# Kernel tuning notes

Measured on AMD Instinct MI355X. Metric: run time of the kernel, lower is better.

Reference implementation:

```python
import jax, jax.numpy as jnp
import numpy as np

N = 100000   # nodes
E = 1600000  # edges
F = 128      # in = hidden channels
L = 4        # num GCN layers
G = 512      # graphs in batch
OUT = 10     # classes
EPS = 1e-5


def setup_inputs() -> dict:
    key = jax.random.key(0)
    ks = jax.random.split(key, 12)
    x = jax.random.normal(ks[0], (N, F), dtype=jnp.float32)
    edge_index = jax.random.randint(ks[1], (2, E), 0, N, dtype=jnp.int64)
    batch = jnp.sort(jax.random.randint(ks[2], (N,), 0, G, dtype=jnp.int64))
    s = 1.0 / np.sqrt(F)
    Ws = jax.random.uniform(ks[3], (L, F, F), jnp.float32, -s, s)
    bs = jax.random.uniform(ks[4], (L, F), jnp.float32, -s, s)
    gammas = jnp.ones((L, F), jnp.float32)
    betas = jnp.zeros((L, F), jnp.float32)
    s1 = 1.0 / np.sqrt(F * L)
    W1 = jax.random.uniform(ks[5], (F * L, F), jnp.float32, -s1, s1)
    b1 = jax.random.uniform(ks[6], (F,), jnp.float32, -s1, s1)
    g1 = jnp.ones((F,), jnp.float32)
    bt1 = jnp.zeros((F,), jnp.float32)
    s2 = 1.0 / np.sqrt(F)
    W2 = jax.random.uniform(ks[7], (F, OUT), jnp.float32, -s2, s2)
    b2 = jax.random.uniform(ks[8], (OUT,), jnp.float32, -s2, s2)
    return {"x": x, "edge_index": edge_index, "batch": batch, "Ws": Ws, "bs": bs,
            "gammas": gammas, "betas": betas, "W1": W1, "b1": b1, "g1": g1,
            "bt1": bt1, "W2": W2, "b2": b2}


def _batch_norm(x, g, b):
    # training-mode BatchNorm1d over the node dim (biased variance)
    mu = jnp.mean(x, axis=0)
    var = jnp.var(x, axis=0)
    return (x - mu) * jax.lax.rsqrt(var + EPS) * g + b


def reference(x, edge_index, batch, Ws, bs, gammas, betas, W1, b1, g1, bt1, W2, b2):
    row, col = edge_index[0], edge_index[1]
    # GCN normalization (add_self_loops=False since normalize=True)
    deg = jax.ops.segment_sum(jnp.ones((E,), x.dtype), col, num_segments=N)
    dinv = jnp.where(deg > 0, jax.lax.rsqrt(deg), 0.0)
    norm = dinv[row] * dinv[col]  # [E]
    pooled = []
    h = x
    for t in range(L):
        hw = h @ Ws[t]                                    # [N, F]
        msg = norm[:, None] * hw[row]                     # gather  [E, F]
        h = jax.ops.segment_sum(msg, col, num_segments=N) + bs[t]  # scatter [N, F]
        h = jax.nn.relu(h)
        h = _batch_norm(h, gammas[t], betas[t])
        pooled.append(jax.ops.segment_sum(h, batch, num_segments=G))  # [G, F]
    z = jnp.concatenate(pooled, axis=1)                   # [G, L*F]
    z = z @ W1 + b1
    z = _batch_norm(z, g1, bt1)
    z = jax.nn.relu(z)
    return z @ W2 + b2                                    # [G, OUT]
```

## Files before the change

### kernel.cpp

```cpp
#include <hip/hip_runtime.h>

#define NN 100000
#define EE 1600000
#define FF 128
#define LL 4
#define GG 512
#define OUTC 10
#define EPSF 1e-5f
#define NSCB ((NN + 255) / 256)

#define NPW 8
#define AGG_WAVES ((NN + NPW - 1) / NPW)
#define AGG_BLOCKS ((AGG_WAVES + 3) / 4)

typedef __attribute__((ext_vector_type(8))) short short8;
typedef __attribute__((ext_vector_type(4))) float f32x4;

__device__ inline unsigned bf16rne(float f) {
  unsigned u = __float_as_uint(f);
  return (u + 0x7fffu + ((u >> 16) & 1u)) >> 16;
}
__device__ inline unsigned packbf(float lo, float hi) {
  return bf16rne(lo) | (bf16rne(hi) << 16);
}
__device__ inline float bflo(unsigned u) { return __uint_as_float(u << 16); }
__device__ inline float bfhi(unsigned u) { return __uint_as_float(u & 0xffff0000u); }


__global__ __launch_bounds__(256) void k_deg(const int* __restrict__ col, int* __restrict__ deg) {
  int e = blockIdx.x * 256 + threadIdx.x;
  if (e < EE) atomicAdd(&deg[col[e]], 1);
}

__global__ __launch_bounds__(256) void k_bsum(const int* __restrict__ deg,
                                              int* __restrict__ bsum,
                                              float* __restrict__ dinv) {
  int i = blockIdx.x * 256 + threadIdx.x;
  int v = (i < NN) ? deg[i] : 0;
  if (i < NN) dinv[i] = v > 0 ? rsqrtf((float)v) : 0.0f;
#pragma unroll
  for (int off = 32; off > 0; off >>= 1) v += __shfl_down(v, off, 64);
  __shared__ int ws[4];
  if ((threadIdx.x & 63) == 0) ws[threadIdx.x >> 6] = v;
  __syncthreads();
  if (threadIdx.x == 0) bsum[blockIdx.x] = ws[0] + ws[1] + ws[2] + ws[3];
}

__global__ __launch_bounds__(256) void k_rowptr(const int* __restrict__ deg,
                                                const int* __restrict__ bsum,
                                                int* __restrict__ rowptr) {
  __shared__ int sb[512];
  __shared__ int sd[256];
  const int t = threadIdx.x;
  sb[t]       = (t < NSCB) ? bsum[t] : 0;
  sb[t + 256] = (t + 256 < NSCB) ? bsum[t + 256] : 0;
  __syncthreads();
#pragma unroll
  for (int off = 1; off < 512; off <<= 1) {
    int v0 = (t >= off) ? sb[t - off] : 0;
    int v1 = sb[t + 256 - off];
    __syncthreads();
    sb[t] += v0;
    sb[t + 256] += v1;
    __syncthreads();
  }
  const int bpre = (blockIdx.x == 0) ? 0 : sb[blockIdx.x - 1];
  const int i = blockIdx.x * 256 + t;
  const int d = (i < NN) ? deg[i] : 0;
  sd[t] = d;
  __syncthreads();
#pragma unroll
  for (int off = 1; off < 256; off <<= 1) {
    int v = (t >= off) ? sd[t - off] : 0;
    __syncthreads();
    sd[t] += v;
    __syncthreads();
  }
  if (i < NN) rowptr[i] = bpre + sd[t] - d;
  if (blockIdx.x == 0 && t == 0) rowptr[NN] = EE;
}

__global__ __launch_bounds__(256) void k_fill(const int* __restrict__ ei,
                                              const int* __restrict__ rowptr,
                                              int* __restrict__ cnt,
                                              const float* __restrict__ dinv,
                                              int2* __restrict__ ecw) {
  int e = blockIdx.x * 256 + threadIdx.x;
  if (e >= EE) return;
  int r = ei[e];
  int cl = ei[EE + e];
  int slot = rowptr[cl] + atomicAdd(&cnt[cl], 1);
  ecw[slot] = make_int2(r, __float_as_int(dinv[r] * dinv[cl]));
}


__global__ __launch_bounds__(256) void k_cvt(const float* __restrict__ x,
                                             const int* __restrict__ batch,
                                             unsigned* __restrict__ Ab,
                                             int* __restrict__ gstart) {
  int i = blockIdx.x * 256 + threadIdx.x;
  if (i < NN * 64) {
    float2 v = *(const float2*)(x + (size_t)i * 2);
    Ab[i] = packbf(v.x, v.y);
  }
  if (i < NN) {
    int b = batch[i];
    if (i == 0) {
      for (int g = 0; g <= b; ++g) gstart[g] = 0;
    } else {
      int bp = batch[i - 1];
      for (int g = bp + 1; g <= b; ++g) gstart[g] = i;
    }
    if (i == NN - 1) {
      for (int g = b + 1; g <= GG; ++g) gstart[g] = NN;
    }
  }
}

__global__ __launch_bounds__(256) void k_wcvt(const float* __restrict__ W,
                                              uint4* __restrict__ Wf) {
  int tid = blockIdx.x * 256 + threadIdx.x;
  int lane = tid & 63;
  int which = (tid >> 6) & 1;
  int ct = (tid >> 7) & 7;
  int kc = tid >> 10;
  int n = ct * 16 + (lane & 15);
  int k0 = kc * 32 + (lane >> 4) * 8;
  unsigned h[8];
#pragma unroll
  for (int j = 0; j < 8; ++j) {
    float w = W[(k0 + j) * 128 + n];
    unsigned hb = bf16rne(w);
    if (which == 0) {
      h[j] = hb;
    } else {
      float hf = __uint_as_float(hb << 16);
      h[j] = bf16rne(w - hf);
    }
  }
  uint4 o;
  o.x = h[0] | (h[1] << 16);
  o.y = h[2] | (h[3] << 16);
  o.z = h[4] | (h[5] << 16);
  o.w = h[6] | (h[7] << 16);
  Wf[tid] = o;
}

__global__ __launch_bounds__(256) void k_post(const float* __restrict__ bnbuf,
                                              const float* __restrict__ gamma,
                                              const float* __restrict__ beta,
                                              float* __restrict__ bnsc,
                                              const float* __restrict__ Wnext,
                                              uint4* __restrict__ Wf,
                                              float* __restrict__ baseo) {
  __shared__ float ssc[256];
  const int t = threadIdx.x;
  if (t < 128) {
    float mu = bnbuf[t] * (1.0f / NN);
    float var = bnbuf[128 + t] * (1.0f / NN) - mu * mu;
    float inv = rsqrtf(var + EPSF);
    float sc = gamma[t] * inv;
    float sh = beta[t] - mu * sc;
    ssc[t] = sc;
    ssc[128 + t] = sh;
    if (blockIdx.x == 0) {
      bnsc[t] = sc;
      bnsc[128 + t] = sh;
    }
  }
  __syncthreads();
  if (gridDim.x == 1) return;
  if (blockIdx.x < 16) {
    int tid = blockIdx.x * 256 + t;
    int lane = tid & 63;
    int which = (tid >> 6) & 1;
    int ct = (tid >> 7) & 7;
    int kc = tid >> 10;
    int n = ct * 16 + (lane & 15);
    int k0 = kc * 32 + (lane >> 4) * 8;
    unsigned h[8];
#pragma unroll
    for (int j = 0; j < 8; ++j) {
      float w = Wnext[(k0 + j) * 128 + n] * ssc[k0 + j];
      unsigned hb = bf16rne(w);
      if (which == 0) {
        h[j] = hb;
      } else {
        float hf = __uint_as_float(hb << 16);
        h[j] = bf16rne(w - hf);
      }
    }
    uint4 o;
    o.x = h[0] | (h[1] << 16);
    o.y = h[2] | (h[3] << 16);
    o.z = h[4] | (h[5] << 16);
    o.w = h[6] | (h[7] << 16);
    Wf[tid] = o;
  } else if (t < 128) {
    float acc = 0.f;
    for (int k = 0; k < 128; ++k) acc = fmaf(ssc[128 + k], Wnext[k * 128 + t], acc);
    baseo[t] = acc;
  }
}

__global__ __launch_bounds__(256) void k_mm(const unsigned* __restrict__ Ab,
                                            const uint4* __restrict__ Wf,
                                            unsigned* __restrict__ Bb) {
  const int lane = threadIdx.x & 63;
  const int w = threadIdx.x >> 6;
  const int quad = lane >> 4;
  const int m = lane & 15;
  const int rowbase = blockIdx.x * 64 + w * 16;
  const int arow = min(rowbase + m, NN - 1);
  const uint4* A4 = (const uint4*)Ab;
  f32x4 acc[8];
#pragma unroll
  for (int ct = 0; ct < 8; ++ct) acc[ct] = (f32x4){0.f, 0.f, 0.f, 0.f};
#pragma unroll
  for (int kc = 0; kc < 4; ++kc) {
    uint4 av = A4[arow * 16 + kc * 4 + quad];
    short8 af = *(short8*)&av;
#pragma unroll
    for (int ct = 0; ct < 8; ++ct) {
      uint4 bh = Wf[((kc * 8 + ct) * 2 + 0) * 64 + lane];
      uint4 bl = Wf[((kc * 8 + ct) * 2 + 1) * 64 + lane];
      acc[ct] = __builtin_amdgcn_mfma_f32_16x16x32_bf16(af, *(short8*)&bh, acc[ct], 0, 0, 0);
      acc[ct] = __builtin_amdgcn_mfma_f32_16x16x32_bf16(af, *(short8*)&bl, acc[ct], 0, 0, 0);
    }
  }
#pragma unroll
  for (int ct = 0; ct < 8; ++ct) {
#pragma unroll
    for (int r = 0; r < 4; ++r) {
      float v = acc[ct][r];
      float vo = __shfl_xor(v, 1);
      int row = rowbase + quad * 4 + r;
      if ((lane & 1) == 0 && row < NN) {
        Bb[row * 64 + ct * 8 + (m >> 1)] = packbf(v, vo);
      }
    }
  }
}

__global__ __launch_bounds__(256) void k_agg(const unsigned* __restrict__ Bb,
                                             const int* __restrict__ rowptr,
                                             const int2* __restrict__ ecw,
                                             const float* __restrict__ bias,
                                             const float* __restrict__ base,
                                             const int* __restrict__ batch,
                                             unsigned* __restrict__ Ar,
                                             float* __restrict__ bnbuf,
                                             float* __restrict__ pooledt) {
  const int lane = threadIdx.x & 63;
  const int wave = threadIdx.x >> 6;
  const int c = lane * 2;
  const int gwave = blockIdx.x * 4 + wave;
  const int n0 = gwave * NPW;
  const float2 bv = *(const float2*)(bias + c);
  const float2 basev = *(const float2*)(base + c);
  float s0 = 0.f, s1 = 0.f, q0 = 0.f, q1 = 0.f;
  __shared__ int srp[4][NPW + 1];
  __shared__ int2 sstage[4][64];
  if (n0 < NN) {
    const int nn = min(NPW, NN - n0);
    if (lane <= nn) srp[wave][lane] = rowptr[n0 + lane];
    int bsp = (lane < nn) ? batch[n0 + lane] : 0;
    float ax0 = 0.f, ax1 = 0.f, ay0 = 0.f, ay1 = 0.f, sw = 0.f;
    float px = 0.f, py = 0.f;
    int gprev = -1;
    auto finalize = [&](int node) {
      float rx = fmaxf(fmaf(sw, basev.x, ax0 + ax1) + bv.x, 0.f);
      float ry = fmaxf(fmaf(sw, basev.y, ay0 + ay1) + bv.y, 0.f);
      Ar[(size_t)(n0 + node) * 64 + lane] = packbf(rx, ry);
      s0 += rx; s1 += ry;
      q0 = fmaf(rx, rx, q0); q1 = fmaf(ry, ry, q1);
      int g = __shfl(bsp, node);
      if (g != gprev) {
        if (gprev >= 0) {
          atomicAdd(&pooledt[(size_t)gprev * 512 + c], px);
          atomicAdd(&pooledt[(size_t)gprev * 512 + c + 1], py);
        }
        gprev = g; px = 0.f; py = 0.f;
      }
      px += rx; py += ry;
      ax0 = 0.f; ax1 = 0.f; ay0 = 0.f; ay1 = 0.f; sw = 0.f;
    };
    const int beg = __builtin_amdgcn_readfirstlane(srp[wave][0]);
    const int endall = __builtin_amdgcn_readfirstlane(srp[wave][nn]);
    int cn = 0;
    while (cn < nn && __builtin_amdgcn_readfirstlane(srp[wave][cn + 1]) == beg) {
      finalize(cn);
      ++cn;
    }
    int nend = (cn < nn) ? __builtin_amdgcn_readfirstlane(srp[wave][cn + 1]) : 0x7fffffff;
    int2 stage = (beg + lane < endall) ? ecw[beg + lane] : make_int2(0, 0);
    for (int base_e = beg; base_e < endall; base_e += 64) {
      sstage[wave][lane] = stage;
      const int nb = base_e + 64;
      if (nb < endall) {
        stage = (nb + lane < endall) ? ecw[nb + lane] : make_int2(0, 0);
      }
      int2 ewA[16], ewB[16];
#pragma unroll
      for (int j = 0; j < 16; ++j) ewA[j] = sstage[wave][j];

#define PROC(G, CUR, NXT, PREF)                                               \
  if (base_e + (G) * 16 < endall) {                                           \
    if (PREF) {                                                               \
      _Pragma("unroll")                                                       \
      for (int j = 0; j < 16; ++j) NXT[j] = sstage[wave][((G) + 1) * 16 + j]; \
    }                                                                         \
    unsigned us[16];                                                          \
    _Pragma("unroll")                                                         \
    for (int j = 0; j < 16; ++j) {                                            \
      const int sj = __builtin_amdgcn_readfirstlane(CUR[j].x);                \
      us[j] = Bb[((size_t)(unsigned)sj << 6) + (unsigned)lane];               \
    }                                                                         \
    _Pragma("unroll")                                                         \
    for (int j = 0; j < 16; ++j) {                                            \
      const float wj = __int_as_float(CUR[j].y);                              \
      sw += wj;                                                               \
      if (j & 1) {                                                            \
        ax1 = fmaf(wj, bflo(us[j]), ax1);                                     \
        ay1 = fmaf(wj, bfhi(us[j]), ay1);                                     \
      } else {                                                                \
        ax0 = fmaf(wj, bflo(us[j]), ax0);                                     \
        ay0 = fmaf(wj, bfhi(us[j]), ay0);                                     \
      }                                                                       \
      const int e1 = base_e + (G) * 16 + j + 1;                               \
      if (e1 == nend) {                                                       \
        finalize(cn); ++cn;                                                   \
        nend = (cn < nn) ? __builtin_amdgcn_readfirstlane(srp[wave][cn + 1])  \
                         : 0x7fffffff;                                        \
        while (cn < nn && nend == e1) {                                       \
          finalize(cn); ++cn;                                                 \
          nend = (cn < nn)                                                    \
                     ? __builtin_amdgcn_readfirstlane(srp[wave][cn + 1])      \
                     : 0x7fffffff;                                            \
        }                                                                     \
      }                                                                       \
    }                                                                         \
  }

      PROC(0, ewA, ewB, true)
      PROC(1, ewB, ewA, true)
      PROC(2, ewA, ewB, true)
      PROC(3, ewB, ewA, false)
#undef PROC
    }
    if (gprev >= 0) {
      atomicAdd(&pooledt[(size_t)gprev * 512 + c], px);
      atomicAdd(&pooledt[(size_t)gprev * 512 + c + 1], py);
    }
  }
  __shared__ float sred[4][256];
  sred[wave][c] = s0;
  sred[wave][c + 1] = s1;
  sred[wave][128 + c] = q0;
  sred[wave][128 + c + 1] = q1;
  __syncthreads();
  const int t = threadIdx.x;
  float tot = sred[0][t] + sred[1][t] + sred[2][t] + sred[3][t];
  atomicAdd(&bnbuf[t], tot);
}


__global__ __launch_bounds__(128) void k_z1(const float* __restrict__ S,
                                            const float* __restrict__ bnscL,
                                            const int* __restrict__ gstart,
                                            const float* __restrict__ W1,
                                            const float* __restrict__ b1,
                                            float* __restrict__ z1) {
  __shared__ float sp[512];
  const int g = blockIdx.x;
  const float cntg = (float)(gstart[g + 1] - gstart[g]);
  for (int i = threadIdx.x; i < 512; i += 128) {
    int t = i >> 7, ch = i & 127;
    sp[i] = fmaf(bnscL[t * 256 + ch], S[(size_t)g * 512 + i], cntg * bnscL[t * 256 + 128 + ch]);
  }
  __syncthreads();
  const int c = threadIdx.x;
  float acc = b1[c];
  for (int j = 0; j < 512; ++j) acc = fmaf(sp[j], W1[j * 128 + c], acc);
  z1[(size_t)g * 128 + c] = acc;
}

__global__ __launch_bounds__(128) void k_zstat(const float* __restrict__ z1,
                                               const float* __restrict__ g1,
                                               const float* __restrict__ bt1,
                                               float* __restrict__ zsc) {
  const int c = threadIdx.x;
  float s = 0.f, q = 0.f;
  for (int g = 0; g < GG; ++g) {
    float v = z1[g * 128 + c];
    s += v;
    q = fmaf(v, v, q);
  }
  float mu = s * (1.0f / GG);
  float var = q * (1.0f / GG) - mu * mu;
  float inv = rsqrtf(var + EPSF);
  float sc = g1[c] * inv;
  zsc[c] = sc;
  zsc[128 + c] = bt1[c] - mu * sc;
}

__global__ __launch_bounds__(128) void k_out(const float* __restrict__ z1,
                                             const float* __restrict__ zsc,
                                             const float* __restrict__ W2,
                                             const float* __restrict__ b2,
                                             float* __restrict__ out) {
  __shared__ float zr[128];
  const int g = blockIdx.x;
  const int c = threadIdx.x;
  zr[c] = fmaxf(fmaf(z1[(size_t)g * 128 + c], zsc[c], zsc[128 + c]), 0.f);
  __syncthreads();
  if (c < OUTC) {
    float acc = b2[c];
    for (int k = 0; k < 128; ++k) acc = fmaf(zr[k], W2[k * OUTC + c], acc);
    out[(size_t)g * OUTC + c] = acc;
  }
}


extern "C" void kernel_launch(void* const* d_in, const int* in_sizes, int n_in,
                              void* d_out, int out_size, void* d_ws, size_t ws_size,
                              hipStream_t stream) {
  const float* x      = (const float*)d_in[0];
  const int*   ei     = (const int*)d_in[1];
  const int*   batch  = (const int*)d_in[2];
  const float* Ws     = (const float*)d_in[3];
  const float* bs     = (const float*)d_in[4];
  const float* gammas = (const float*)d_in[5];
  const float* betas  = (const float*)d_in[6];
  const float* W1     = (const float*)d_in[7];
  const float* b1     = (const float*)d_in[8];
  const float* g1     = (const float*)d_in[9];
  const float* bt1    = (const float*)d_in[10];
  const float* W2     = (const float*)d_in[11];
  const float* b2     = (const float*)d_in[12];
  float* out = (float*)d_out;

  char* ws = (char*)d_ws;
  size_t off = 0;
  auto alloc = [&](size_t bytes) -> void* {
    void* p = ws + off;
    off = (off + bytes + 255) & ~(size_t)255;
    return p;
  };
  int*   deg    = (int*)alloc((size_t)NN * 4);
  int*   cnt    = (int*)alloc((size_t)NN * 4);
  float* bnbuf  = (float*)alloc((size_t)LL * 256 * 4);
  float* pooled = (float*)alloc((size_t)GG * 512 * 4);
  float* zbase  = (float*)alloc(128 * 4);
  size_t zero_bytes = off;
  unsigned* Ar     = (unsigned*)alloc((size_t)NN * 64 * 4);
  unsigned* Ab     = (unsigned*)alloc((size_t)NN * 64 * 4);
  unsigned* Bb     = (unsigned*)alloc((size_t)NN * 64 * 4);
  int2*     ecw    = (int2*)alloc((size_t)EE * 8);
  float*    dinv   = (float*)alloc((size_t)NN * 4);
  int*      rowptr = (int*)alloc((size_t)(NN + 1) * 4);
  int*      bsum   = (int*)alloc((size_t)NSCB * 4);
  int*      gstart = (int*)alloc((size_t)(GG + 1) * 4);
  uint4*    Wf     = (uint4*)alloc((size_t)4096 * 16);
  float*    z1     = (float*)alloc((size_t)GG * FF * 4);
  float*    bnscL  = (float*)alloc((size_t)LL * 256 * 4);
  float*    basebf = (float*)alloc(128 * 4);
  float*    zsc    = (float*)alloc(256 * 4);
  (void)ws_size; (void)in_sizes; (void)n_in; (void)out_size;

  hipMemsetAsync(d_ws, 0, zero_bytes, stream);

  k_deg<<<(EE + 255) / 256, 256, 0, stream>>>(ei + EE, deg);
  k_bsum<<<NSCB, 256, 0, stream>>>(deg, bsum, dinv);
  k_rowptr<<<NSCB, 256, 0, stream>>>(deg, bsum, rowptr);
  k_fill<<<(EE + 255) / 256, 256, 0, stream>>>(ei, rowptr, cnt, dinv, ecw);
  k_cvt<<<(NN * 64 + 255) / 256, 256, 0, stream>>>(x, batch, Ab, gstart);
  k_wcvt<<<16, 256, 0, stream>>>(Ws, Wf);

  for (int t = 0; t < LL; ++t) {
    k_mm<<<(NN + 63) / 64, 256, 0, stream>>>(t == 0 ? Ab : Ar, Wf, Bb);
    k_agg<<<AGG_BLOCKS, 256, 0, stream>>>(Bb, rowptr, ecw, bs + t * FF,
                                          t == 0 ? zbase : basebf, batch,
                                          Ar, bnbuf + t * 256, pooled + t * FF);
    if (t < LL - 1) {
      k_post<<<17, 256, 0, stream>>>(bnbuf + t * 256, gammas + t * FF, betas + t * FF,
                                     bnscL + t * 256, Ws + (size_t)(t + 1) * 16384,
                                     Wf, basebf);
    } else {
      k_post<<<1, 256, 0, stream>>>(bnbuf + t * 256, gammas + t * FF, betas + t * FF,
                                    bnscL + t * 256, nullptr, nullptr, nullptr);
    }
  }

  k_z1<<<GG, 128, 0, stream>>>(pooled, bnscL, gstart, W1, b1, z1);
  k_zstat<<<1, 128, 0, stream>>>(z1, g1, bt1, zsc);
  k_out<<<GG, 128, 0, stream>>>(z1, zsc, W2, b2, out);
}
```

Baseline: 910.3 us.

## Double nodes per wave, simplify edge staging loop, parallelize zstat reduction

The aggregation kernel now gives each wave 16 destination nodes instead of 8, which halves the number of blocks. Its ping-pong register prefetch macro is replaced by a plain unrolled loop that reads each 16-edge group from shared memory right before issuing its gathers. The final BN statistics kernel goes from 1 block of 128 threads to 1024 threads and combines the partial sums through shared memory. The intent is less per-wave overhead and a shorter serial reduction, at the cost of fewer waves for hiding latency and the loss of the overlapped staging loads.

```diff
diff --git a/kernel.cpp b/kernel.cpp
--- a/kernel.cpp
+++ b/kernel.cpp
@@ -9,7 +9,7 @@
 #define EPSF 1e-5f
 #define NSCB ((NN + 255) / 256)
 
-#define NPW 8
+#define NPW 16
 #define AGG_WAVES ((NN + NPW - 1) / NPW)
 #define AGG_BLOCKS ((AGG_WAVES + 3) / 4)
 
@@ -300,53 +300,42 @@
       if (nb < endall) {
         stage = (nb + lane < endall) ? ecw[nb + lane] : make_int2(0, 0);
       }
-      int2 ewA[16], ewB[16];
-#pragma unroll
-      for (int j = 0; j < 16; ++j) ewA[j] = sstage[wave][j];
-
-#define PROC(G, CUR, NXT, PREF)                                               \
-  if (base_e + (G) * 16 < endall) {                                           \
-    if (PREF) {                                                               \
-      _Pragma("unroll")                                                       \
-      for (int j = 0; j < 16; ++j) NXT[j] = sstage[wave][((G) + 1) * 16 + j]; \
-    }                                                                         \
-    unsigned us[16];                                                          \
-    _Pragma("unroll")                                                         \
-    for (int j = 0; j < 16; ++j) {                                            \
-      const int sj = __builtin_amdgcn_readfirstlane(CUR[j].x);                \
-      us[j] = Bb[((size_t)(unsigned)sj << 6) + (unsigned)lane];               \
-    }                                                                         \
-    _Pragma("unroll")                                                         \
-    for (int j = 0; j < 16; ++j) {                                            \
-      const float wj = __int_as_float(CUR[j].y);                              \
-      sw += wj;                                                               \
-      if (j & 1) {                                                            \
-        ax1 = fmaf(wj, bflo(us[j]), ax1);                                     \
-        ay1 = fmaf(wj, bfhi(us[j]), ay1);                                     \
-      } else {                                                                \
-        ax0 = fmaf(wj, bflo(us[j]), ax0);                                     \
-        ay0 = fmaf(wj, bfhi(us[j]), ay0);                                     \
-      }                                                                       \
-      const int e1 = base_e + (G) * 16 + j + 1;                               \
-      if (e1 == nend) {                                                       \
-        finalize(cn); ++cn;                                                   \
-        nend = (cn < nn) ? __builtin_amdgcn_readfirstlane(srp[wave][cn + 1])  \
-                         : 0x7fffffff;                                        \
-        while (cn < nn && nend == e1) {                                       \
-          finalize(cn); ++cn;                                                 \
-          nend = (cn < nn)                                                    \
-                     ? __builtin_amdgcn_readfirstlane(srp[wave][cn + 1])      \
-                     : 0x7fffffff;                                            \
-        }                                                                     \
-      }                                                                       \
-    }                                                                         \
-  }
-
-      PROC(0, ewA, ewB, true)
-      PROC(1, ewB, ewA, true)
-      PROC(2, ewA, ewB, true)
-      PROC(3, ewB, ewA, false)
-#undef PROC
+#pragma unroll
+      for (int g = 0; g < 4; ++g) {
+        if (base_e + g * 16 < endall) {
+          int2 ew[16]; unsigned us[16];
+#pragma unroll
+          for (int j = 0; j < 16; ++j) ew[j] = sstage[wave][g * 16 + j];
+#pragma unroll
+          for (int j = 0; j < 16; ++j) {
+            const int sj = __builtin_amdgcn_readfirstlane(ew[j].x);
+            us[j] = Bb[((size_t)(unsigned)sj << 6) + (unsigned)lane];
+          }
+#pragma unroll
+          for (int j = 0; j < 16; ++j) {
+            const float wj = __int_as_float(ew[j].y);
+            sw += wj;
+            if (j & 1) {
+              ax1 = fmaf(wj, bflo(us[j]), ax1);
+              ay1 = fmaf(wj, bfhi(us[j]), ay1);
+            } else {
+              ax0 = fmaf(wj, bflo(us[j]), ax0);
+              ay0 = fmaf(wj, bfhi(us[j]), ay0);
+            }
+            const int e1 = base_e + g * 16 + j + 1;
+            if (e1 == nend) {
+              finalize(cn);
+              ++cn;
+              nend = (cn < nn) ? __builtin_amdgcn_readfirstlane(srp[wave][cn + 1]) : 0x7fffffff;
+              while (cn < nn && nend == e1) {
+                finalize(cn);
+                ++cn;
+                nend = (cn < nn) ? __builtin_amdgcn_readfirstlane(srp[wave][cn + 1]) : 0x7fffffff;
+              }
+            }
+          }
+        }
+      }
     }
     if (gprev >= 0) {
       atomicAdd(&pooledt[(size_t)gprev * 512 + c], px);
@@ -385,23 +374,35 @@
   z1[(size_t)g * 128 + c] = acc;
 }
 
-__global__ __launch_bounds__(128) void k_zstat(const float* __restrict__ z1,
-                                               const float* __restrict__ g1,
-                                               const float* __restrict__ bt1,
-                                               float* __restrict__ zsc) {
-  const int c = threadIdx.x;
+__global__ __launch_bounds__(1024) void k_zstat(const float* __restrict__ z1,
+                                                const float* __restrict__ g1,
+                                                const float* __restrict__ bt1,
+                                                float* __restrict__ zsc) {
+  const int t = threadIdx.x;
+  const int c = t & 127;
+  const int gr = t >> 7;
   float s = 0.f, q = 0.f;
-  for (int g = 0; g < GG; ++g) {
-    float v = z1[g * 128 + c];
+  for (int g = gr; g < GG; g += 8) {
+    float v = z1[(size_t)g * 128 + c];
     s += v;
     q = fmaf(v, v, q);
   }
-  float mu = s * (1.0f / GG);
-  float var = q * (1.0f / GG) - mu * mu;
-  float inv = rsqrtf(var + EPSF);
-  float sc = g1[c] * inv;
-  zsc[c] = sc;
-  zsc[128 + c] = bt1[c] - mu * sc;
+  __shared__ float ss[8][128];
+  __shared__ float sq[8][128];
+  ss[gr][c] = s;
+  sq[gr][c] = q;
+  __syncthreads();
+  if (t < 128) {
+    float st = 0.f, qt = 0.f;
+#pragma unroll
+    for (int i = 0; i < 8; ++i) { st += ss[i][c]; qt += sq[i][c]; }
+    float mu = st * (1.0f / GG);
+    float var = qt * (1.0f / GG) - mu * mu;
+    float inv = rsqrtf(var + EPSF);
+    float sc = g1[c] * inv;
+    zsc[c] = sc;
+    zsc[128 + c] = bt1[c] - mu * sc;
+  }
 }
 
 __global__ __launch_bounds__(128) void k_out(const float* __restrict__ z1,
@@ -493,6 +494,6 @@
   }
 
   k_z1<<<GG, 128, 0, stream>>>(pooled, bnscL, gstart, W1, b1, z1);
-  k_zstat<<<1, 128, 0, stream>>>(z1, g1, bt1, zsc);
+  k_zstat<<<1, 1024, 0, stream>>>(z1, g1, bt1, zsc);
   k_out<<<GG, 128, 0, stream>>>(z1, zsc, W2, b2, out);
 }
```

Measured after the change: 781.3 us. -14.2%, faster.
